# Optimization experiments

Hardware: AMD Instinct MI355X
Metric: run time of the kernel (lower is better)

The kernel has to match this reference:

```python
import jax, jax.numpy as jnp
import numpy as np

GAMMA = 1.0
ALPHA = 0.5
EMBED_DIM = 256
N = 8192
M = 8192


def setup_inputs() -> dict:
    key = jax.random.key(0)
    k1, k2, k3, k4 = jax.random.split(key, 4)
    a = jax.random.normal(k1, (N, EMBED_DIM), dtype=jnp.float32)
    b = jax.random.normal(k2, (M, EMBED_DIM), dtype=jnp.float32)
    # torch.nn.Linear default init: U(-1/sqrt(fan_in), 1/sqrt(fan_in))
    lim = 1.0 / np.sqrt(EMBED_DIM)
    Wq = jax.random.uniform(k3, (EMBED_DIM, EMBED_DIM), jnp.float32, -lim, lim)
    Wk = jax.random.uniform(k4, (EMBED_DIM, EMBED_DIM), jnp.float32, -lim, lim)
    return {"a": a, "b": b, "Wq": Wq, "Wk": Wk}


def reference(a, b, Wq, Wk):
    # Vectorized Gram matrix of HybridKernelMethod.forward over all (a_i, b_j) pairs.
    inv_sqrt_d = np.float32(1.0 / np.sqrt(EMBED_DIM))
    ab = a @ b.T                                           # [N, M] cross dot products
    # RBF part: ||a_i - b_j||^2 = ||a_i||^2 + ||b_j||^2 - 2 a_i.b_j
    sq = (jnp.sum(a * a, axis=-1)[:, None]
          + jnp.sum(b * b, axis=-1)[None, :] - 2.0 * ab)
    rbf_sim = jnp.exp(-GAMMA * sq)                         # [N, M]
    # Attention part: per pair, q k^T is a 1x1 matrix, so softmax == 1 exactly.
    q = a @ Wq.T                                           # [N, D]
    k = b @ Wk.T                                           # [M, D]
    s = (q @ k.T) * inv_sqrt_d                             # [N, M] scores
    scores = jax.nn.softmax(s[..., None], axis=-1)[..., 0]  # all-ones, faithful to 1x1 softmax
    attn_sim = scores * ab                                 # sum((scores @ v) * x) == scores * (a.b)
    return (1.0 - ALPHA) * rbf_sim + ALPHA * attn_sim      # [N, M] Gram matrix
```

## Files before the change

kernel.cpp:

```cpp
#include <hip/hip_runtime.h>
#include <stdint.h>

#define DIM 256
#define NR 8192
#define BM 128
#define BN 128
#define BK 64
#define TPB 8
#define GRID 512

typedef __bf16 bf16x8 __attribute__((ext_vector_type(8)));
typedef float  f32x16 __attribute__((ext_vector_type(16)));
typedef float  f32x4  __attribute__((ext_vector_type(4)));

#define MEMFENCE asm volatile("" ::: "memory")
#define WAITV(N) asm volatile("s_waitcnt vmcnt(" #N ")" ::: "memory")
#define BAR __builtin_amdgcn_s_barrier()

__device__ __forceinline__ unsigned short f2bf_rne(float f) {
    unsigned int u = __float_as_uint(f);
    u += 0x7FFFu + ((u >> 16) & 1u);
    return (unsigned short)(u >> 16);
}

__global__ void prep_kernel(const float* __restrict__ a,
                            const float* __restrict__ b,
                            unsigned short* __restrict__ aB,
                            unsigned short* __restrict__ bB,
                            float* __restrict__ na,
                            float* __restrict__ nb) {
    const int w = threadIdx.x >> 6;
    const int l = threadIdx.x & 63;
    const int blk = blockIdx.x;
    const float* src; unsigned short* dst; float* nrm; int row;
    if (blk < 2048) { src = a; dst = aB; nrm = na; row = blk * 4 + w; }
    else            { src = b; dst = bB; nrm = nb; row = (blk - 2048) * 4 + w; }
    const float4 v = reinterpret_cast<const float4*>(src + (size_t)row * DIM)[l];
    float ss = v.x * v.x + v.y * v.y + v.z * v.z + v.w * v.w;
#pragma unroll
    for (int off = 32; off > 0; off >>= 1) ss += __shfl_down(ss, off);
    if (l == 0) nrm[row] = ss;
    ushort4 o = make_ushort4(f2bf_rne(v.x), f2bf_rne(v.y), f2bf_rne(v.z), f2bf_rne(v.w));
    reinterpret_cast<ushort4*>(dst + (size_t)row * DIM)[l] = o;
}

#define STAGE(row0_, kt_, buf_)                                                   \
    do {                                                                          \
        _Pragma("unroll")                                                         \
        for (int it_ = 0; it_ < 4; ++it_) {                                       \
            __builtin_amdgcn_global_load_lds(                                     \
                (const __attribute__((address_space(1))) void*)(aB +              \
                    (size_t)((row0_) + rowIt[it_]) * DIM + (kt_) * BK + colIt[it_]), \
                (__attribute__((address_space(3))) void*)&sA[buf_][(w * 4 + it_) * 512], \
                16, 0, 0);                                                        \
        }                                                                         \
        _Pragma("unroll")                                                         \
        for (int it_ = 0; it_ < 4; ++it_) {                                       \
            __builtin_amdgcn_global_load_lds(                                     \
                (const __attribute__((address_space(1))) void*)(bB +              \
                    (size_t)(col0 + rowIt[it_]) * DIM + (kt_) * BK + colIt[it_]), \
                (__attribute__((address_space(3))) void*)&sB[buf_][(w * 4 + it_) * 512], \
                16, 0, 0);                                                        \
        }                                                                         \
    } while (0)

#define COMPUTE(buf_)                                                             \
    do {                                                                          \
        __builtin_amdgcn_s_setprio(1);                                            \
        _Pragma("unroll")                                                         \
        for (int ks_ = 0; ks_ < 4; ++ks_) {                                       \
            bf16x8 af[2], bfv[2];                                                 \
            _Pragma("unroll")                                                     \
            for (int mi_ = 0; mi_ < 2; ++mi_)                                     \
                af[mi_] = *(const bf16x8*)((const char*)&sA[buf_][0] +            \
                    baseA[mi_] + ((XA[mi_] ^ (ks_ << 1)) << 4));                  \
            _Pragma("unroll")                                                     \
            for (int ni_ = 0; ni_ < 2; ++ni_)                                     \
                bfv[ni_] = *(const bf16x8*)((const char*)&sB[buf_][0] +           \
                    baseB[ni_] + ((XB[ni_] ^ (ks_ << 1)) << 4));                  \
            _Pragma("unroll")                                                     \
            for (int mi_ = 0; mi_ < 2; ++mi_)                                     \
                _Pragma("unroll")                                                 \
                for (int ni_ = 0; ni_ < 2; ++ni_)                                 \
                    acc[mi_][ni_] = __builtin_amdgcn_mfma_f32_32x32x16_bf16(      \
                        af[mi_], bfv[ni_], acc[mi_][ni_], 0, 0, 0);               \
        }                                                                         \
        __builtin_amdgcn_s_setprio(0);                                            \
    } while (0)

#define STORE_CHUNK(c_, base_)                                                    \
    do {                                                                          \
        const int mi_ = (c_) >> 1, ni_ = (c_) & 1;                                \
        const int prow_ = (base_) + wr * 64 + mi_ * 32 + 4 * hi;                  \
        const int pcol_ = col0 + wc * 64 + ni_ * 32 + lr;                         \
        _Pragma("unroll")                                                         \
        for (int tt_ = 0; tt_ < 16; ++tt_) {                                      \
            const int q_ = tt_ & 3, p_ = tt_ >> 2;                                \
            out[(size_t)(prow_ + 8 * p_ + q_) * 8192 + pcol_] = outB[c_][tt_];    \
        }                                                                         \
    } while (0)

__global__ __launch_bounds__(256, 2) void gemm_kernel(
        const unsigned short* __restrict__ aB,
        const unsigned short* __restrict__ bB,
        const float* __restrict__ na,
        const float* __restrict__ nb,
        float* __restrict__ out) {
    __shared__ unsigned short sA[2][8192];
    __shared__ unsigned short sB[2][8192];
    __shared__ float sNA[1024];

    const int t = threadIdx.x;
    const int w = t >> 6, l = t & 63;
    const int wr = w >> 1, wc = w & 1;
    const int hi = l >> 5, lr = l & 31;

    const int bx = (int)blockIdx.x & 63;
    const int bb = (int)blockIdx.x >> 6;
    const int col0 = bx * BN;

    int rowIt[4], colIt[4];
#pragma unroll
    for (int it = 0; it < 4; ++it) {
        int G = (w * 4 + it) * 64 + l;
        int rp = G >> 4, pos = G & 15;
        int c2 = pos ^ (rp & 15);
        rowIt[it] = 2 * rp + (c2 >> 3);
        colIt[it] = (c2 & 7) * 8;
    }
    int baseA[2], XA[2], baseB[2], XB[2];
#pragma unroll
    for (int mi = 0; mi < 2; ++mi) {
        int r = wr * 64 + mi * 32 + lr;
        baseA[mi] = (r >> 1) * 256;
        XA[mi] = (((r & 1) * 8) | hi) ^ ((r >> 1) & 15);
        int rb = wc * 64 + mi * 32 + lr;
        baseB[mi] = (rb >> 1) * 256;
        XB[mi] = (((rb & 1) * 8) | hi) ^ ((rb >> 1) & 15);
    }

    float nbv[2];
#pragma unroll
    for (int ni = 0; ni < 2; ++ni) nbv[ni] = nb[col0 + wc * 64 + ni * 32 + lr];

    float outB[4][16];

    const f32x4 naIn = *(const f32x4*)&na[(bb + (t >> 5) * 8) * 128 + (t & 31) * 4];
    {
        const int r0 = bb * BM;
        STAGE(r0, 0, 0);
        STAGE(r0, 1, 1);
    }
    *(f32x4*)&sNA[(t >> 5) * 128 + (t & 31) * 4] = naIn;
    asm volatile("s_waitcnt lgkmcnt(0)" ::: "memory");
    MEMFENCE;

    for (int ti = 0; ti < TPB; ++ti) {
        const int row0 = (bb + ti * 8) * BM;
        f32x16 acc[2][2];
#pragma unroll
        for (int mi = 0; mi < 2; ++mi)
#pragma unroll
            for (int ni = 0; ni < 2; ++ni) acc[mi][ni] = (f32x16)0.0f;

        if (ti <= 1) { WAITV(8); } else { WAITV(40); }
        BAR; MEMFENCE;
        COMPUTE(0);
        MEMFENCE; BAR; MEMFENCE;
        STAGE(row0, 2, 0);
        MEMFENCE;
        if (ti > 0) STORE_CHUNK(0, row0 - 1024);
        MEMFENCE;

        if (ti == 0) { WAITV(8); } else if (ti == 1) { WAITV(24); } else { WAITV(40); }
        BAR; MEMFENCE;
        COMPUTE(1);
        MEMFENCE; BAR; MEMFENCE;
        STAGE(row0, 3, 1);
        MEMFENCE;
        if (ti > 0) STORE_CHUNK(1, row0 - 1024);
        MEMFENCE;

        if (ti == 0) { WAITV(8); } else { WAITV(40); }
        BAR; MEMFENCE;
        COMPUTE(0);
        MEMFENCE; BAR; MEMFENCE;
        if (ti < TPB - 1) STAGE(row0 + 1024, 0, 0);
        MEMFENCE;
        if (ti > 0) STORE_CHUNK(2, row0 - 1024);
        MEMFENCE;

        if (ti == 0) { WAITV(8); } else if (ti == TPB - 1) { WAITV(32); } else { WAITV(40); }
        BAR; MEMFENCE;
        COMPUTE(1);
        MEMFENCE; BAR; MEMFENCE;
        if (ti < TPB - 1) STAGE(row0 + 1024, 1, 1);
        MEMFENCE;
        if (ti > 0) STORE_CHUNK(3, row0 - 1024);
        MEMFENCE;

#pragma unroll
        for (int mi = 0; mi < 2; ++mi)
#pragma unroll
            for (int ni = 0; ni < 2; ++ni)
#pragma unroll
                for (int p = 0; p < 4; ++p) {
                    const f32x4 nv = *(const f32x4*)&sNA[ti * 128 + wr * 64 + mi * 32 + 8 * p + 4 * hi];
#pragma unroll
                    for (int q = 0; q < 4; ++q) {
                        const float dot = acc[mi][ni][p * 4 + q];
                        const float sq = nv[q] + nbv[ni] - 2.0f * dot;
                        outB[mi * 2 + ni][p * 4 + q] = 0.5f * __expf(-sq) + 0.5f * dot;
                    }
                }
        MEMFENCE;
    }

    {
        const int base = (bb + 56) * BM;
#pragma unroll
        for (int c = 0; c < 4; ++c) STORE_CHUNK(c, base);
    }
}

__global__ void naive_kernel(const float* __restrict__ a,
                             const float* __restrict__ b,
                             float* __restrict__ out) {
    const size_t idx = (size_t)blockIdx.x * 256 + threadIdx.x;
    const int i = (int)(idx >> 13);
    const int j = (int)(idx & 8191);
    float dot = 0.f, naa = 0.f, nbb = 0.f;
    for (int k = 0; k < DIM; ++k) {
        const float x = a[(size_t)i * DIM + k];
        const float y = b[(size_t)j * DIM + k];
        dot += x * y; naa += x * x; nbb += y * y;
    }
    const float sq = naa + nbb - 2.0f * dot;
    out[idx] = 0.5f * __expf(-sq) + 0.5f * dot;
}

extern "C" void kernel_launch(void* const* d_in, const int* in_sizes, int n_in,
                              void* d_out, int out_size, void* d_ws, size_t ws_size,
                              hipStream_t stream) {
    const float* a = (const float*)d_in[0];
    const float* b = (const float*)d_in[1];
    float* out = (float*)d_out;

    const size_t bf_bytes = (size_t)NR * DIM * sizeof(unsigned short);
    const size_t nrm_bytes = (size_t)NR * sizeof(float);
    const size_t need = 2 * bf_bytes + 2 * nrm_bytes;

    if (ws_size >= need) {
        unsigned short* aBf = (unsigned short*)d_ws;
        unsigned short* bBf = (unsigned short*)((char*)d_ws + bf_bytes);
        float* na = (float*)((char*)d_ws + 2 * bf_bytes);
        float* nb = (float*)((char*)d_ws + 2 * bf_bytes + nrm_bytes);

        prep_kernel<<<4096, 256, 0, stream>>>(a, b, aBf, bBf, na, nb);
        gemm_kernel<<<GRID, 256, 0, stream>>>(aBf, bBf, na, nb, out);
    } else {
        naive_kernel<<<((size_t)NR * NR) / 256, 256, 0, stream>>>(a, b, out);
    }
}
```

Baseline: 79.28 us.

## Use one 128x128 tile per block with BK=32 and shuffle-transposed vector stores

Replaces the persistent 512-block schedule, where each block walks 8 row tiles and overlaps stores with the next tile's loads, with a 4096-block grid where each block computes a single 128x128 tile. The K step drops to 32 with smaller LDS buffers and a simpler swizzle, and launch bounds rise to 4 blocks per CU for occupancy. The epilogue transposes accumulator values across lanes with xor shuffles so each lane writes a contiguous float4 instead of scalar stores. The cost is losing the explicit store/load overlap, paying a prologue and epilogue per tile, and more barriers per unit of work.

Result: slower. 87.17 us (+10.0%).

```diff
diff --git a/kernel.cpp b/kernel.cpp
--- a/kernel.cpp
+++ b/kernel.cpp
@@ -5,9 +5,8 @@
 #define NR 8192
 #define BM 128
 #define BN 128
-#define BK 64
-#define TPB 8
-#define GRID 512
+#define BK 32
+#define GRID 4096
 
 typedef __bf16 bf16x8 __attribute__((ext_vector_type(8)));
 typedef float  f32x16 __attribute__((ext_vector_type(16)));
@@ -44,22 +43,22 @@
     reinterpret_cast<ushort4*>(dst + (size_t)row * DIM)[l] = o;
 }
 
-#define STAGE(row0_, kt_, buf_)                                                   \
+#define STAGE(kt_, buf_)                                                          \
     do {                                                                          \
         _Pragma("unroll")                                                         \
-        for (int it_ = 0; it_ < 4; ++it_) {                                       \
+        for (int it_ = 0; it_ < 2; ++it_) {                                       \
             __builtin_amdgcn_global_load_lds(                                     \
                 (const __attribute__((address_space(1))) void*)(aB +              \
-                    (size_t)((row0_) + rowIt[it_]) * DIM + (kt_) * BK + colIt[it_]), \
-                (__attribute__((address_space(3))) void*)&sA[buf_][(w * 4 + it_) * 512], \
+                    (size_t)(row0 + w * 32 + it_ * 16 + rQ) * DIM + (kt_) * BK + cOf), \
+                (__attribute__((address_space(3))) void*)&sA[buf_][(w * 2 + it_) * 512], \
                 16, 0, 0);                                                        \
         }                                                                         \
         _Pragma("unroll")                                                         \
-        for (int it_ = 0; it_ < 4; ++it_) {                                       \
+        for (int it_ = 0; it_ < 2; ++it_) {                                       \
             __builtin_amdgcn_global_load_lds(                                     \
                 (const __attribute__((address_space(1))) void*)(bB +              \
-                    (size_t)(col0 + rowIt[it_]) * DIM + (kt_) * BK + colIt[it_]), \
-                (__attribute__((address_space(3))) void*)&sB[buf_][(w * 4 + it_) * 512], \
+                    (size_t)(col0 + w * 32 + it_ * 16 + rQ) * DIM + (kt_) * BK + cOf), \
+                (__attribute__((address_space(3))) void*)&sB[buf_][(w * 2 + it_) * 512], \
                 16, 0, 0);                                                        \
         }                                                                         \
     } while (0)
@@ -68,16 +67,16 @@
     do {                                                                          \
         __builtin_amdgcn_s_setprio(1);                                            \
         _Pragma("unroll")                                                         \
-        for (int ks_ = 0; ks_ < 4; ++ks_) {                                       \
+        for (int ks_ = 0; ks_ < 2; ++ks_) {                                       \
             bf16x8 af[2], bfv[2];                                                 \
             _Pragma("unroll")                                                     \
             for (int mi_ = 0; mi_ < 2; ++mi_)                                     \
                 af[mi_] = *(const bf16x8*)((const char*)&sA[buf_][0] +            \
-                    baseA[mi_] + ((XA[mi_] ^ (ks_ << 1)) << 4));                  \
+                    baseA[mi_] + (((ks_ << 1) ^ XA[mi_]) << 4));                  \
             _Pragma("unroll")                                                     \
             for (int ni_ = 0; ni_ < 2; ++ni_)                                     \
                 bfv[ni_] = *(const bf16x8*)((const char*)&sB[buf_][0] +           \
-                    baseB[ni_] + ((XB[ni_] ^ (ks_ << 1)) << 4));                  \
+                    baseB[ni_] + (((ks_ << 1) ^ XB[ni_]) << 4));                  \
             _Pragma("unroll")                                                     \
             for (int mi_ = 0; mi_ < 2; ++mi_)                                     \
                 _Pragma("unroll")                                                 \
@@ -88,27 +87,16 @@
         __builtin_amdgcn_s_setprio(0);                                            \
     } while (0)
 
-#define STORE_CHUNK(c_, base_)                                                    \
-    do {                                                                          \
-        const int mi_ = (c_) >> 1, ni_ = (c_) & 1;                                \
-        const int prow_ = (base_) + wr * 64 + mi_ * 32 + 4 * hi;                  \
-        const int pcol_ = col0 + wc * 64 + ni_ * 32 + lr;                         \
-        _Pragma("unroll")                                                         \
-        for (int tt_ = 0; tt_ < 16; ++tt_) {                                      \
-            const int q_ = tt_ & 3, p_ = tt_ >> 2;                                \
-            out[(size_t)(prow_ + 8 * p_ + q_) * 8192 + pcol_] = outB[c_][tt_];    \
-        }                                                                         \
-    } while (0)
-
-__global__ __launch_bounds__(256, 2) void gemm_kernel(
+__global__ __launch_bounds__(256, 4) void gemm_kernel(
         const unsigned short* __restrict__ aB,
         const unsigned short* __restrict__ bB,
         const float* __restrict__ na,
         const float* __restrict__ nb,
         float* __restrict__ out) {
-    __shared__ unsigned short sA[2][8192];
-    __shared__ unsigned short sB[2][8192];
-    __shared__ float sNA[1024];
+    __shared__ unsigned short sA[2][4096];
+    __shared__ unsigned short sB[2][4096];
+    __shared__ float sNA[128];
+    __shared__ float sNB[128];
 
     const int t = threadIdx.x;
     const int w = t >> 6, l = t & 63;
@@ -116,110 +104,84 @@
     const int hi = l >> 5, lr = l & 31;
 
     const int bx = (int)blockIdx.x & 63;
-    const int bb = (int)blockIdx.x >> 6;
+    const int by = (int)blockIdx.x >> 6;
     const int col0 = bx * BN;
-
-    int rowIt[4], colIt[4];
-#pragma unroll
-    for (int it = 0; it < 4; ++it) {
-        int G = (w * 4 + it) * 64 + l;
-        int rp = G >> 4, pos = G & 15;
-        int c2 = pos ^ (rp & 15);
-        rowIt[it] = 2 * rp + (c2 >> 3);
-        colIt[it] = (c2 & 7) * 8;
-    }
+    const int row0 = by * BM;
+
+    const int rQ = l >> 2;
+    const int cOf = ((l & 3) ^ ((l >> 3) & 3)) * 8;
+
     int baseA[2], XA[2], baseB[2], XB[2];
 #pragma unroll
     for (int mi = 0; mi < 2; ++mi) {
-        int r = wr * 64 + mi * 32 + lr;
-        baseA[mi] = (r >> 1) * 256;
-        XA[mi] = (((r & 1) * 8) | hi) ^ ((r >> 1) & 15);
-        int rb = wc * 64 + mi * 32 + lr;
-        baseB[mi] = (rb >> 1) * 256;
-        XB[mi] = (((rb & 1) * 8) | hi) ^ ((rb >> 1) & 15);
-    }
-
-    float nbv[2];
-#pragma unroll
-    for (int ni = 0; ni < 2; ++ni) nbv[ni] = nb[col0 + wc * 64 + ni * 32 + lr];
-
-    float outB[4][16];
-
-    const f32x4 naIn = *(const f32x4*)&na[(bb + (t >> 5) * 8) * 128 + (t & 31) * 4];
-    {
-        const int r0 = bb * BM;
-        STAGE(r0, 0, 0);
-        STAGE(r0, 1, 1);
-    }
-    *(f32x4*)&sNA[(t >> 5) * 128 + (t & 31) * 4] = naIn;
+        const int r = wr * 64 + mi * 32 + lr;
+        baseA[mi] = r * 64;
+        XA[mi] = hi ^ ((r >> 1) & 3);
+        const int rb = wc * 64 + mi * 32 + lr;
+        baseB[mi] = rb * 64;
+        XB[mi] = hi ^ ((rb >> 1) & 3);
+    }
+
+    f32x4 nIn;
+    if (t < 32)      nIn = *(const f32x4*)&na[row0 + t * 4];
+    else if (t < 64) nIn = *(const f32x4*)&nb[col0 + (t - 32) * 4];
+    STAGE(0, 0);
+    STAGE(1, 1);
+    if (t < 32)      *(f32x4*)&sNA[t * 4] = nIn;
+    else if (t < 64) *(f32x4*)&sNB[(t - 32) * 4] = nIn;
     asm volatile("s_waitcnt lgkmcnt(0)" ::: "memory");
     MEMFENCE;
 
-    for (int ti = 0; ti < TPB; ++ti) {
-        const int row0 = (bb + ti * 8) * BM;
-        f32x16 acc[2][2];
-#pragma unroll
-        for (int mi = 0; mi < 2; ++mi)
-#pragma unroll
-            for (int ni = 0; ni < 2; ++ni) acc[mi][ni] = (f32x16)0.0f;
-
-        if (ti <= 1) { WAITV(8); } else { WAITV(40); }
+    f32x16 acc[2][2];
+#pragma unroll
+    for (int mi = 0; mi < 2; ++mi)
+#pragma unroll
+        for (int ni = 0; ni < 2; ++ni) acc[mi][ni] = (f32x16)0.0f;
+
+#pragma unroll
+    for (int p = 0; p < 8; ++p) {
+        if (p == 7) { WAITV(0); } else { WAITV(4); }
         BAR; MEMFENCE;
-        COMPUTE(0);
-        MEMFENCE; BAR; MEMFENCE;
-        STAGE(row0, 2, 0);
+        COMPUTE(p & 1);
         MEMFENCE;
-        if (ti > 0) STORE_CHUNK(0, row0 - 1024);
-        MEMFENCE;
-
-        if (ti == 0) { WAITV(8); } else if (ti == 1) { WAITV(24); } else { WAITV(40); }
-        BAR; MEMFENCE;
-        COMPUTE(1);
-        MEMFENCE; BAR; MEMFENCE;
-        STAGE(row0, 3, 1);
-        MEMFENCE;
-        if (ti > 0) STORE_CHUNK(1, row0 - 1024);
-        MEMFENCE;
-
-        if (ti == 0) { WAITV(8); } else { WAITV(40); }
-        BAR; MEMFENCE;
-        COMPUTE(0);
-        MEMFENCE; BAR; MEMFENCE;
-        if (ti < TPB - 1) STAGE(row0 + 1024, 0, 0);
-        MEMFENCE;
-        if (ti > 0) STORE_CHUNK(2, row0 - 1024);
-        MEMFENCE;
-
-        if (ti == 0) { WAITV(8); } else if (ti == TPB - 1) { WAITV(32); } else { WAITV(40); }
-        BAR; MEMFENCE;
-        COMPUTE(1);
-        MEMFENCE; BAR; MEMFENCE;
-        if (ti < TPB - 1) STAGE(row0 + 1024, 1, 1);
-        MEMFENCE;
-        if (ti > 0) STORE_CHUNK(3, row0 - 1024);
-        MEMFENCE;
-
-#pragma unroll
-        for (int mi = 0; mi < 2; ++mi)
-#pragma unroll
-            for (int ni = 0; ni < 2; ++ni)
-#pragma unroll
-                for (int p = 0; p < 4; ++p) {
-                    const f32x4 nv = *(const f32x4*)&sNA[ti * 128 + wr * 64 + mi * 32 + 8 * p + 4 * hi];
-#pragma unroll
-                    for (int q = 0; q < 4; ++q) {
-                        const float dot = acc[mi][ni][p * 4 + q];
-                        const float sq = nv[q] + nbv[ni] - 2.0f * dot;
-                        outB[mi * 2 + ni][p * 4 + q] = 0.5f * __expf(-sq) + 0.5f * dot;
-                    }
+        if (p < 6) {
+            BAR; MEMFENCE;
+            STAGE(p + 2, p & 1);
+            MEMFENCE;
+        }
+    }
+
+    const int m4 = l & 3;
+    const int colT = col0 + wc * 64 + (lr >> 2) * 4;
+#pragma unroll
+    for (int ni = 0; ni < 2; ++ni) {
+        const float nbv = sNB[wc * 64 + ni * 32 + lr];
+#pragma unroll
+        for (int mi = 0; mi < 2; ++mi) {
+#pragma unroll
+            for (int p = 0; p < 4; ++p) {
+                const f32x4 nv = *(const f32x4*)&sNA[wr * 64 + mi * 32 + 8 * p + 4 * hi];
+                float av[4];
+#pragma unroll
+                for (int q = 0; q < 4; ++q) {
+                    const float dot = acc[mi][ni][p * 4 + q];
+                    const float sq = nv[q] + nbv - 2.0f * dot;
+                    av[q] = 0.5f * __expf(-sq) + 0.5f * dot;
                 }
-        MEMFENCE;
-    }
-
-    {
-        const int base = (bb + 56) * BM;
-#pragma unroll
-        for (int c = 0; c < 4; ++c) STORE_CHUNK(c, base);
+                float tv;
+                tv = __shfl_xor((m4 & 1) ? av[0] : av[1], 1);
+                if (m4 & 1) av[0] = tv; else av[1] = tv;
+                tv = __shfl_xor((m4 & 1) ? av[2] : av[3], 1);
+                if (m4 & 1) av[2] = tv; else av[3] = tv;
+                tv = __shfl_xor((m4 & 2) ? av[0] : av[2], 2);
+                if (m4 & 2) av[0] = tv; else av[2] = tv;
+                tv = __shfl_xor((m4 & 2) ? av[1] : av[3], 2);
+                if (m4 & 2) av[1] = tv; else av[3] = tv;
+                const int row = row0 + wr * 64 + mi * 32 + 8 * p + 4 * hi + m4;
+                f32x4 st; st[0] = av[0]; st[1] = av[1]; st[2] = av[2]; st[3] = av[3];
+                *(f32x4*)&out[(size_t)row * 8192 + colT + ni * 32] = st;
+            }
+        }
     }
 }
 
```
